# Performance work log

Hardware: AMD Instinct MI355X
Metric: run time of the kernel (lower is better)

Reference implementation:

```python
import jax, jax.numpy as jnp
import numpy as np

C_IN = 3072
C_OUT = 1024
MAJ = 3  # majority_size


def setup_inputs() -> dict:
    key = jax.random.key(0)
    k1, k2 = jax.random.split(key)
    x = jax.random.normal(k1, (256, C_IN), dtype=jnp.float32)
    stdv = 1.0 / np.sqrt(C_OUT * C_IN)
    weight = jax.random.uniform(k2, (C_OUT, C_IN), dtype=jnp.float32, minval=-stdv, maxval=stdv)
    return {"input": x, "weight": weight}


def reference(input, weight):
    B = input.shape[0]
    G = C_IN // MAJ  # number of majority groups
    # Deterministic binarization (sign), as in Binarize(..., 'det')
    xb = jnp.sign(input)            # [B, C_IN]
    wb = jnp.sign(weight)           # [C_OUT, C_IN]
    # Grouped products: inter[b,c,g] = sum_k xb[b,g,k] * wb[c,g,k]
    # (equivalent to einsum('bj,cj->bcj') followed by reshape+sum over groups of 3)
    xg = xb.reshape(B, G, MAJ)
    wg = wb.reshape(C_OUT, G, MAJ)
    inter = jnp.einsum('bgk,cgk->bcg', xg, wg)  # [B, C_OUT, G]
    # Majority vote: clamp group sums to [-1, 1], sum across groups, scale by 2.25
    out = jnp.sum(jnp.clip(inter, -1.0, 1.0), axis=2) * 2.25  # [B, C_OUT]
    return out
```

## Files before the change

kernel.cpp:

```cpp
#include <hip/hip_runtime.h>
#include <stdint.h>

#define B_SZ 256
#define C_IN 3072
#define C_OUT 1024
#define WORDS 16

__global__ __launch_bounds__(256) void pack_x(const float* __restrict__ x,
                                              uint64_t* __restrict__ xpk) {
    int wid  = blockIdx.x * 4 + (threadIdx.x >> 6);
    int lane = threadIdx.x & 63;
    int b    = wid >> 4;
    int word = wid & 15;
    const float* row = x + (size_t)b * C_IN + word * 192;
    uint64_t* dst = xpk + (size_t)b * 96 + word * 6;
    float v0 = row[3 * lane + 0];
    float v1 = row[3 * lane + 1];
    float v2 = row[3 * lane + 2];
    uint64_t p0 = __ballot(v0 > 0.0f), z0 = __ballot(v0 != 0.0f);
    uint64_t p1 = __ballot(v1 > 0.0f), z1 = __ballot(v1 != 0.0f);
    uint64_t p2 = __ballot(v2 > 0.0f), z2 = __ballot(v2 != 0.0f);
    if (lane == 0) {
        dst[0] = p0; dst[1] = p1; dst[2] = p2;
        dst[3] = z0; dst[4] = z1; dst[5] = z2;
    }
}

__global__ __launch_bounds__(256) void pack_w(const float* __restrict__ w,
                                              uint64_t* __restrict__ wpk) {
    int wid  = blockIdx.x * 4 + (threadIdx.x >> 6);
    int lane = threadIdx.x & 63;
    int c    = wid >> 4;
    int word = wid & 15;
    const float* row = w + (size_t)c * C_IN + word * 192;
    float v0 = row[3 * lane + 0];
    float v1 = row[3 * lane + 1];
    float v2 = row[3 * lane + 2];
    uint64_t p0 = __ballot(v0 > 0.0f), z0 = __ballot(v0 != 0.0f);
    uint64_t p1 = __ballot(v1 > 0.0f), z1 = __ballot(v1 != 0.0f);
    uint64_t p2 = __ballot(v2 > 0.0f), z2 = __ballot(v2 != 0.0f);
    if (lane == 0) {
        uint64_t* base = wpk + (size_t)word * 6 * C_OUT + c;
        base[0 * C_OUT] = p0; base[1 * C_OUT] = p1; base[2 * C_OUT] = p2;
        base[3 * C_OUT] = z0; base[4 * C_OUT] = z1; base[5 * C_OUT] = z2;
    }
}

#define BT 2
__global__ __launch_bounds__(256) void maj_main(const uint64_t* __restrict__ wpk,
                                                const uint64_t* __restrict__ xpk,
                                                float* __restrict__ out) {
    __shared__ uint64_t xs[BT * 96];
    int tid = threadIdx.x;
    int bt  = blockIdx.x >> 2;
    int ct  = blockIdx.x & 3;
    int b0  = bt * BT;
    int c   = ct * 256 + tid;

    for (int i = tid; i < BT * 96; i += 256)
        xs[i] = xpk[(size_t)b0 * 96 + i];
    __syncthreads();

    int accP[BT], accN[BT];
#pragma unroll
    for (int i = 0; i < BT; ++i) { accP[i] = 0; accN[i] = 0; }

    for (int word = 0; word < WORDS; ++word) {
        const uint64_t* wb = wpk + (size_t)word * 6 * C_OUT + c;
        uint64_t WP0 = wb[0 * C_OUT], WP1 = wb[1 * C_OUT], WP2 = wb[2 * C_OUT];
        uint64_t WZ0 = wb[3 * C_OUT], WZ1 = wb[4 * C_OUT], WZ2 = wb[5 * C_OUT];
#pragma unroll
        for (int bi = 0; bi < BT; ++bi) {
            const uint64_t* xr = &xs[bi * 96 + word * 6];
            uint64_t t0 = xr[0] ^ WP0, z0 = xr[3] & WZ0;
            uint64_t t1 = xr[1] ^ WP1, z1 = xr[4] & WZ1;
            uint64_t t2 = xr[2] ^ WP2, z2 = xr[5] & WZ2;
            uint64_t P0 = z0 & ~t0, N0 = z0 & t0;
            uint64_t P1 = z1 & ~t1, N1 = z1 & t1;
            uint64_t P2 = z2 & ~t2, N2 = z2 & t2;
            uint64_t a0 = P0 ^ P1 ^ P2;
            uint64_t a1 = (P0 & P1) | (P2 & (P0 | P1));
            uint64_t c0 = N0 ^ N1 ^ N2;
            uint64_t c1 = (N0 & N1) | (N2 & (N0 | N1));
            uint64_t ne1 = a1 ^ c1;
            uint64_t gt = (a1 & ~c1) | (~ne1 & (a0 & ~c0));
            uint64_t lt = (c1 & ~a1) | (~ne1 & (c0 & ~a0));
            accP[bi] += __popcll(gt);
            accN[bi] += __popcll(lt);
        }
    }
#pragma unroll
    for (int bi = 0; bi < BT; ++bi)
        out[(size_t)(b0 + bi) * C_OUT + c] = 2.25f * (float)(accP[bi] - accN[bi]);
}

extern "C" void kernel_launch(void* const* d_in, const int* in_sizes, int n_in,
                              void* d_out, int out_size, void* d_ws, size_t ws_size,
                              hipStream_t stream) {
    const float* x = (const float*)d_in[0];
    const float* w = (const float*)d_in[1];
    float* out = (float*)d_out;

    uint64_t* wpk = (uint64_t*)d_ws;
    uint64_t* xpk = (uint64_t*)((char*)d_ws + (size_t)WORDS * 6 * C_OUT * 8);

    pack_x<<<(B_SZ * WORDS) / 4, 256, 0, stream>>>(x, xpk);
    pack_w<<<(C_OUT * WORDS) / 4, 256, 0, stream>>>(w, wpk);
    maj_main<<<(B_SZ / BT) * 4, 256, 0, stream>>>(wpk, xpk, out);
}
```

Measured before the change: 79.09 us.

## Fuse pack kernels, interleave packed weight layout, drop LDS staging of x

Merges the x and weight packing kernels into one launch. Stores packed weights with the six words per output channel contiguous, so the pack writes are contiguous and the main kernel loads each channel's words together. The main kernel now reads packed x directly from global memory instead of staging it through shared memory with a barrier. It also simplifies the P/N mask computation and unrolls the word loop by two. The main-kernel weight loads become strided per thread rather than fully coalesced per word, which is the main trade-off.

```diff
diff --git a/kernel.cpp b/kernel.cpp
--- a/kernel.cpp
+++ b/kernel.cpp
@@ -5,15 +5,28 @@
 #define C_IN 3072
 #define C_OUT 1024
 #define WORDS 16
+#define XW (B_SZ * WORDS)
+#define WW (C_OUT * WORDS)
 
-__global__ __launch_bounds__(256) void pack_x(const float* __restrict__ x,
-                                              uint64_t* __restrict__ xpk) {
+
+__global__ __launch_bounds__(256) void pack_both(const float* __restrict__ x,
+                                                 const float* __restrict__ w,
+                                                 uint64_t* __restrict__ xpk,
+                                                 uint64_t* __restrict__ wpk) {
     int wid  = blockIdx.x * 4 + (threadIdx.x >> 6);
     int lane = threadIdx.x & 63;
-    int b    = wid >> 4;
-    int word = wid & 15;
-    const float* row = x + (size_t)b * C_IN + word * 192;
-    uint64_t* dst = xpk + (size_t)b * 96 + word * 6;
+    const float* row;
+    uint64_t* dst;
+    if (wid < XW) {
+        int b = wid >> 4, word = wid & 15;
+        row = x + (size_t)b * C_IN + word * 192;
+        dst = xpk + (size_t)b * 96 + word * 6;
+    } else {
+        int id = wid - XW;
+        int c = id >> 4, word = id & 15;
+        row = w + (size_t)c * C_IN + word * 192;
+        dst = wpk + ((size_t)word * C_OUT + c) * 6;
+    }
     float v0 = row[3 * lane + 0];
     float v1 = row[3 * lane + 1];
     float v2 = row[3 * lane + 2];
@@ -26,58 +39,32 @@
     }
 }
 
-__global__ __launch_bounds__(256) void pack_w(const float* __restrict__ w,
-                                              uint64_t* __restrict__ wpk) {
-    int wid  = blockIdx.x * 4 + (threadIdx.x >> 6);
-    int lane = threadIdx.x & 63;
-    int c    = wid >> 4;
-    int word = wid & 15;
-    const float* row = w + (size_t)c * C_IN + word * 192;
-    float v0 = row[3 * lane + 0];
-    float v1 = row[3 * lane + 1];
-    float v2 = row[3 * lane + 2];
-    uint64_t p0 = __ballot(v0 > 0.0f), z0 = __ballot(v0 != 0.0f);
-    uint64_t p1 = __ballot(v1 > 0.0f), z1 = __ballot(v1 != 0.0f);
-    uint64_t p2 = __ballot(v2 > 0.0f), z2 = __ballot(v2 != 0.0f);
-    if (lane == 0) {
-        uint64_t* base = wpk + (size_t)word * 6 * C_OUT + c;
-        base[0 * C_OUT] = p0; base[1 * C_OUT] = p1; base[2 * C_OUT] = p2;
-        base[3 * C_OUT] = z0; base[4 * C_OUT] = z1; base[5 * C_OUT] = z2;
-    }
-}
-
 #define BT 2
 __global__ __launch_bounds__(256) void maj_main(const uint64_t* __restrict__ wpk,
                                                 const uint64_t* __restrict__ xpk,
                                                 float* __restrict__ out) {
-    __shared__ uint64_t xs[BT * 96];
     int tid = threadIdx.x;
     int bt  = blockIdx.x >> 2;
     int ct  = blockIdx.x & 3;
     int b0  = bt * BT;
     int c   = ct * 256 + tid;
 
-    for (int i = tid; i < BT * 96; i += 256)
-        xs[i] = xpk[(size_t)b0 * 96 + i];
-    __syncthreads();
-
     int accP[BT], accN[BT];
 #pragma unroll
     for (int i = 0; i < BT; ++i) { accP[i] = 0; accN[i] = 0; }
 
+#pragma unroll 2
     for (int word = 0; word < WORDS; ++word) {
-        const uint64_t* wb = wpk + (size_t)word * 6 * C_OUT + c;
-        uint64_t WP0 = wb[0 * C_OUT], WP1 = wb[1 * C_OUT], WP2 = wb[2 * C_OUT];
-        uint64_t WZ0 = wb[3 * C_OUT], WZ1 = wb[4 * C_OUT], WZ2 = wb[5 * C_OUT];
+        const uint64_t* wb = wpk + ((size_t)word * C_OUT + c) * 6;
+        uint64_t WP0 = wb[0], WP1 = wb[1], WP2 = wb[2];
+        uint64_t WZ0 = wb[3], WZ1 = wb[4], WZ2 = wb[5];
 #pragma unroll
         for (int bi = 0; bi < BT; ++bi) {
-            const uint64_t* xr = &xs[bi * 96 + word * 6];
-            uint64_t t0 = xr[0] ^ WP0, z0 = xr[3] & WZ0;
-            uint64_t t1 = xr[1] ^ WP1, z1 = xr[4] & WZ1;
-            uint64_t t2 = xr[2] ^ WP2, z2 = xr[5] & WZ2;
-            uint64_t P0 = z0 & ~t0, N0 = z0 & t0;
-            uint64_t P1 = z1 & ~t1, N1 = z1 & t1;
-            uint64_t P2 = z2 & ~t2, N2 = z2 & t2;
+            const uint64_t* xr = xpk + (size_t)(b0 + bi) * 96 + word * 6;
+            uint64_t t0 = xr[0] ^ WP0, t1 = xr[1] ^ WP1, t2 = xr[2] ^ WP2;
+            uint64_t z0 = xr[3] & WZ0, z1 = xr[4] & WZ1, z2 = xr[5] & WZ2;
+            uint64_t N0 = z0 & t0, N1 = z1 & t1, N2 = z2 & t2;
+            uint64_t P0 = z0 ^ N0, P1 = z1 ^ N1, P2 = z2 ^ N2;
             uint64_t a0 = P0 ^ P1 ^ P2;
             uint64_t a1 = (P0 & P1) | (P2 & (P0 | P1));
             uint64_t c0 = N0 ^ N1 ^ N2;
@@ -104,7 +91,6 @@
     uint64_t* wpk = (uint64_t*)d_ws;
     uint64_t* xpk = (uint64_t*)((char*)d_ws + (size_t)WORDS * 6 * C_OUT * 8);
 
-    pack_x<<<(B_SZ * WORDS) / 4, 256, 0, stream>>>(x, xpk);
-    pack_w<<<(C_OUT * WORDS) / 4, 256, 0, stream>>>(w, wpk);
+    pack_both<<<(XW + WW) / 4, 256, 0, stream>>>(x, w, xpk, wpk);
     maj_main<<<(B_SZ / BT) * 4, 256, 0, stream>>>(wpk, xpk, out);
 }
```

New measurement: 74.60 us. 5.7% less time.
